# Kernel tuning notes

Hardware: AMD Instinct MI355X
Metric: run time of the kernel (lower is better)

The kernel has to match this reference:

```python
import jax, jax.numpy as jnp
import numpy as np

# Dimensions derived from Mamba.__init__: d_model=512 -> joint_latent=32, mamb_latent=D=640
NL, D, DIN, DS, DTR, DC = 4, 640, 1280, 16, 40, 4  # n_layer, d_model, d_inner, d_state, dt_rank, d_conv
B, V = 64, 30  # batch, joint-sequence length (repeat_joint_num)


def _rms(x, w, eps=1e-5):
    return x * jax.lax.rsqrt(jnp.mean(x * x, axis=-1, keepdims=True) + eps) * w


def _mamba_block(x, in_w, conv_w, conv_b, xp_w, dt_w, dt_b, A_log, D_skip, out_w):
    # x: [B, V, D]
    u, res = jnp.split(jnp.einsum('bvd,ed->bve', x, in_w), 2, axis=-1)  # each [B,V,DIN]
    # causal depthwise conv1d over V
    xc = jnp.pad(u.transpose(0, 2, 1), ((0, 0), (0, 0), (DC - 1, 0)))  # [B,DIN,V+DC-1]
    xc = jax.lax.conv_general_dilated(xc, conv_w[:, None, :], (1,), 'VALID',
                                      feature_group_count=DIN,
                                      dimension_numbers=('NCH', 'OIH', 'NCH'))
    u = jax.nn.silu(xc.transpose(0, 2, 1) + conv_b)  # [B,V,DIN]
    # input-dependent SSM params
    dbl = jnp.einsum('bvd,ed->bve', u, xp_w)  # [B,V,DTR+2*DS]
    delta, Bm, Cm = jnp.split(dbl, [DTR, DTR + DS], axis=-1)
    delta = jax.nn.softplus(jnp.einsum('bvr,dr->bvd', delta, dt_w) + dt_b)  # [B,V,DIN]
    A = -jnp.exp(A_log)  # [DIN,DS]
    dA = jnp.exp(delta[..., None] * A)                              # [B,V,DIN,DS]
    dBu = delta[..., None] * Bm[:, :, None, :] * u[..., None]       # [B,V,DIN,DS]

    def step(h, t):
        dA_t, dBu_t, C_t = t
        h = dA_t * h + dBu_t                      # [B,DIN,DS]
        return h, jnp.einsum('bds,bs->bd', h, C_t)

    h0 = jnp.zeros((x.shape[0], DIN, DS), x.dtype)
    _, ys = jax.lax.scan(step, h0, (dA.transpose(1, 0, 2, 3),
                                    dBu.transpose(1, 0, 2, 3),
                                    Cm.transpose(1, 0, 2)))
    y = ys.transpose(1, 0, 2) + u * D_skip        # [B,V,DIN]
    return jnp.einsum('bvd,ed->bve', y * jax.nn.silu(res), out_w)


def setup_inputs() -> dict:
    key = jax.random.key(0)
    ks = jax.random.split(key, 10)
    s = 0.02
    return {
        'x': jax.random.normal(ks[0], (B, V, D), jnp.float32),
        'vs': jax.random.randint(ks[1], (B,), 0, V),
        'norm_w': jnp.ones((NL, D), jnp.float32),
        'in_proj_w': s * jax.random.normal(ks[2], (NL, 2 * DIN, D), jnp.float32),
        'conv_w': s * jax.random.normal(ks[3], (NL, DIN, DC), jnp.float32),
        'conv_b': jnp.zeros((NL, DIN), jnp.float32),
        'x_proj_w': s * jax.random.normal(ks[4], (NL, DTR + 2 * DS, DIN), jnp.float32),
        'dt_proj_w': s * jax.random.normal(ks[5], (NL, DIN, DTR), jnp.float32),
        'dt_proj_b': jnp.full((NL, DIN), -4.0, jnp.float32) + 0.1 * jax.random.normal(ks[6], (NL, DIN), jnp.float32),
        'A_log': jnp.tile(jnp.log(jnp.arange(1.0, DS + 1.0, dtype=jnp.float32)), (NL, DIN, 1)),
        'D_skip': jnp.ones((NL, DIN), jnp.float32),
        'out_proj_w': s * jax.random.normal(ks[7], (NL, D, DIN), jnp.float32),
        'norm_f_w': jnp.ones((D,), jnp.float32),
    }


def reference(x, vs, norm_w, in_proj_w, conv_w, conv_b, x_proj_w, dt_proj_w,
              dt_proj_b, A_log, D_skip, out_proj_w, norm_f_w):
    bidx = jnp.arange(x.shape[0])[:, None]
    # batch-wise circular permutation over V (circular_permute_v)
    fwd_idx = (jnp.arange(V)[None, :] + V - vs[:, None]) % V  # [B,V]
    h = x[bidx, fwd_idx]
    for i in range(NL):
        h = h + _mamba_block(_rms(h, norm_w[i]), in_proj_w[i], conv_w[i], conv_b[i],
                             x_proj_w[i], dt_proj_w[i], dt_proj_b[i], A_log[i],
                             D_skip[i], out_proj_w[i])
    h = _rms(h, norm_f_w)
    # reverse_circular_permute_v
    rev_idx = (jnp.arange(V)[None, :] + vs[:, None]) % V
    return h[bidx, rev_idx]
```

## Files before the change

### kernel.cpp

```cpp
#include <hip/hip_runtime.h>
#include <math.h>

#define NLAYER 4
#define DMODEL 640
#define DINNER 1280
#define DSTATE 16
#define DTRANK 40
#define DCONV  4
#define BATCH  64
#define SEQ    30
#define MTOK   (BATCH*SEQ)
#define NPROJ  (2*DINNER)
#define NDBL   (DTRANK+2*DSTATE)
#define NDBLP  80
#define KSEGS  8
#define KSEG   (DINNER/KSEGS)
#define DTKP   64

#define Q1 (NLAYER*NPROJ*DMODEL/4)
#define Q2 (NLAYER*DMODEL*DINNER/4)
#define Q3 (NLAYER*NDBLP*DINNER/4)
#define Q4 (NLAYER*DINNER*DTKP/4)
#define WCTOT (Q1+Q2+Q3+Q4)

typedef unsigned short u16;
typedef __bf16 bf16x8 __attribute__((ext_vector_type(8)));
typedef float  f32x4  __attribute__((ext_vector_type(4)));
typedef unsigned short u16x8 __attribute__((ext_vector_type(8)));

__device__ __forceinline__ float siluf(float x) {
    return x / (1.0f + __expf(-x));
}

__device__ __forceinline__ u16 f2bf(float f) {
    unsigned int u = __float_as_uint(f);
    u += 0x7fffu + ((u >> 16) & 1u);
    return (u16)(u >> 16);
}

__device__ __forceinline__ float bf2f(u16 b) {
    return __uint_as_float(((unsigned int)b) << 16);
}

__global__ void k_permute(const float* __restrict__ x, const int* __restrict__ vs,
                          float* __restrict__ h) {
    int idx = blockIdx.x * blockDim.x + threadIdx.x;
    if (idx >= MTOK * DMODEL) return;
    int d  = idx % DMODEL;
    int mv = idx / DMODEL;
    int v  = mv % SEQ;
    int b  = mv / SEQ;
    int src = (v + SEQ - vs[b]) % SEQ;
    h[idx] = x[(b * SEQ + src) * DMODEL + d];
}

__global__ __launch_bounds__(256)
void k_wconv(const float* __restrict__ in_w, const float* __restrict__ out_w,
             const float* __restrict__ xp_w, const float* __restrict__ dt_w,
             u16* __restrict__ wbi, u16* __restrict__ wbo,
             u16* __restrict__ wbx, u16* __restrict__ wdt) {
    int i = blockIdx.x * 256 + threadIdx.x;
    if (i < Q1) {
        int j = i * 4;
        float4 v = *(const float4*)(in_w + j);
        ushort4 o;
        o.x = f2bf(v.x); o.y = f2bf(v.y); o.z = f2bf(v.z); o.w = f2bf(v.w);
        *(ushort4*)(wbi + j) = o;
    } else if (i < Q1 + Q2) {
        int j = (i - Q1) * 4;
        float4 v = *(const float4*)(out_w + j);
        ushort4 o;
        o.x = f2bf(v.x); o.y = f2bf(v.y); o.z = f2bf(v.z); o.w = f2bf(v.w);
        *(ushort4*)(wbo + j) = o;
    } else if (i < Q1 + Q2 + Q3) {
        int j = (i - Q1 - Q2) * 4;
        int layer = j / (NDBLP * DINNER);
        int rem   = j % (NDBLP * DINNER);
        int r = rem / DINNER, c = rem % DINNER;
        ushort4 o = make_ushort4(0, 0, 0, 0);
        if (r < NDBL) {
            float4 v = *(const float4*)(xp_w + ((size_t)layer * NDBL + r) * DINNER + c);
            o.x = f2bf(v.x); o.y = f2bf(v.y); o.z = f2bf(v.z); o.w = f2bf(v.w);
        }
        *(ushort4*)(wbx + j) = o;
    } else {
        int j = (i - Q1 - Q2 - Q3) * 4;
        int ld = j / DTKP;
        int c  = j % DTKP;
        ushort4 o = make_ushort4(0, 0, 0, 0);
        if (c < DTRANK) {
            float4 v = *(const float4*)(dt_w + (size_t)ld * DTRANK + c);
            o.x = f2bf(v.x); o.y = f2bf(v.y); o.z = f2bf(v.z); o.w = f2bf(v.w);
        }
        *(ushort4*)(wdt + j) = o;
    }
}

__global__ __launch_bounds__(64)
void k_rmsnorm(const float* __restrict__ h, const float* __restrict__ w,
               u16* __restrict__ xn) {
    int m = blockIdx.x;
    int t = threadIdx.x;
    const float* row = h + (size_t)m * DMODEL;
    float2 vv[5];
    float ss = 0.f;
    #pragma unroll
    for (int i = 0; i < 5; ++i) {
        vv[i] = *(const float2*)(row + i * 128 + t * 2);
        ss += vv[i].x * vv[i].x + vv[i].y * vv[i].y;
    }
    #pragma unroll
    for (int o = 32; o > 0; o >>= 1) ss += __shfl_xor(ss, o, 64);
    float sc = rsqrtf(ss / DMODEL + 1e-5f);
    u16* outp = xn + (size_t)m * DMODEL;
    #pragma unroll
    for (int i = 0; i < 5; ++i) {
        int d = i * 128 + t * 2;
        float2 wv = *(const float2*)(w + d);
        ushort2 o;
        o.x = f2bf(vv[i].x * sc * wv.x);
        o.y = f2bf(vv[i].y * sc * wv.y);
        *(ushort2*)(outp + d) = o;
    }
}

__global__ __launch_bounds__(256)
void k_inproj(const u16* __restrict__ A, const u16* __restrict__ W,
              u16* __restrict__ Cb) {
    __shared__ u16 As[2][64 * 64];
    __shared__ u16 Bs[2][128 * 64];
    const int t = threadIdx.x;
    const int w = t >> 6, l = t & 63;
    const int lane15 = l & 15, quad = l >> 4;
    const int wm = w >> 1, wn = w & 1;
    const int m0 = blockIdx.y * 64, n0 = blockIdx.x * 128;

    f32x4 acc[2][4];
    #pragma unroll
    for (int i = 0; i < 2; ++i)
        #pragma unroll
        for (int j = 0; j < 4; ++j)
            acc[i][j] = (f32x4){0.f, 0.f, 0.f, 0.f};

    auto stage = [&](int buf, int k0) {
        #pragma unroll
        for (int q = 0; q < 2; ++q) {
            int c   = q * 256 + t;
            int row = c >> 3;
            int gch = ((c & 7) ^ (row & 7)) * 8;
            const u16* ga = A + (size_t)(m0 + row) * DMODEL + k0 + gch;
            __builtin_amdgcn_global_load_lds(
                (const __attribute__((address_space(1))) void*)ga,
                (__attribute__((address_space(3))) void*)&As[buf][c * 8], 16, 0, 0);
        }
        #pragma unroll
        for (int q = 0; q < 4; ++q) {
            int c   = q * 256 + t;
            int row = c >> 3;
            int gch = ((c & 7) ^ (row & 7)) * 8;
            const u16* gb = W + (size_t)(n0 + row) * DMODEL + k0 + gch;
            __builtin_amdgcn_global_load_lds(
                (const __attribute__((address_space(1))) void*)gb,
                (__attribute__((address_space(3))) void*)&Bs[buf][c * 8], 16, 0, 0);
        }
    };

    auto compute = [&](int buf) {
        #pragma unroll
        for (int ks = 0; ks < 2; ++ks) {
            bf16x8 af[2], bfr[4];
            #pragma unroll
            for (int i = 0; i < 2; ++i) {
                int row = wm * 32 + i * 16 + lane15;
                af[i] = *(const bf16x8*)&As[buf][row * 64 + (((ks * 4 + quad) ^ (row & 7)) * 8)];
            }
            #pragma unroll
            for (int j = 0; j < 4; ++j) {
                int row = wn * 64 + j * 16 + lane15;
                bfr[j] = *(const bf16x8*)&Bs[buf][row * 64 + (((ks * 4 + quad) ^ (row & 7)) * 8)];
            }
            #pragma unroll
            for (int i = 0; i < 2; ++i)
                #pragma unroll
                for (int j = 0; j < 4; ++j)
                    acc[i][j] = __builtin_amdgcn_mfma_f32_16x16x32_bf16(
                        af[i], bfr[j], acc[i][j], 0, 0, 0);
        }
    };

    const int NT = DMODEL / 64;
    stage(0, 0);
    __syncthreads();
    int cur = 0;
    for (int tt = 1; tt < NT; ++tt) {
        stage(cur ^ 1, tt * 64);
        compute(cur);
        __syncthreads();
        cur ^= 1;
    }
    compute(cur);

    #pragma unroll
    for (int i = 0; i < 2; ++i) {
        #pragma unroll
        for (int r = 0; r < 4; ++r) {
            int row = m0 + wm * 32 + i * 16 + quad * 4 + r;
            #pragma unroll
            for (int j = 0; j < 4; ++j) {
                int col = n0 + wn * 64 + j * 16 + lane15;
                Cb[(size_t)row * NPROJ + col] = f2bf(acc[i][j][r]);
            }
        }
    }
}

__global__ __launch_bounds__(128)
void k_outproj(const u16* __restrict__ A, const u16* __restrict__ W,
               const float* __restrict__ resid, float* __restrict__ C) {
    __shared__ u16 As[2][32 * 64];
    __shared__ u16 Bs[2][64 * 64];
    const int t = threadIdx.x;
    const int w = t >> 6, l = t & 63;
    const int lane15 = l & 15, quad = l >> 4;
    const int m0 = blockIdx.y * 32, n0 = blockIdx.x * 64;

    f32x4 acc[2][2];
    #pragma unroll
    for (int i = 0; i < 2; ++i)
        #pragma unroll
        for (int j = 0; j < 2; ++j)
            acc[i][j] = (f32x4){0.f, 0.f, 0.f, 0.f};

    auto stage = [&](int buf, int k0) {
        #pragma unroll
        for (int q = 0; q < 2; ++q) {
            int c   = q * 128 + t;
            int row = c >> 3;
            int gch = ((c & 7) ^ (row & 7)) * 8;
            const u16* ga = A + (size_t)(m0 + row) * DINNER + k0 + gch;
            __builtin_amdgcn_global_load_lds(
                (const __attribute__((address_space(1))) void*)ga,
                (__attribute__((address_space(3))) void*)&As[buf][c * 8], 16, 0, 0);
        }
        #pragma unroll
        for (int q = 0; q < 4; ++q) {
            int c   = q * 128 + t;
            int row = c >> 3;
            int gch = ((c & 7) ^ (row & 7)) * 8;
            const u16* gb = W + (size_t)(n0 + row) * DINNER + k0 + gch;
            __builtin_amdgcn_global_load_lds(
                (const __attribute__((address_space(1))) void*)gb,
                (__attribute__((address_space(3))) void*)&Bs[buf][c * 8], 16, 0, 0);
        }
    };

    auto compute = [&](int buf) {
        #pragma unroll
        for (int ks = 0; ks < 2; ++ks) {
            bf16x8 af[2], bfr[2];
            #pragma unroll
            for (int i = 0; i < 2; ++i) {
                int row = i * 16 + lane15;
                af[i] = *(const bf16x8*)&As[buf][row * 64 + (((ks * 4 + quad) ^ (row & 7)) * 8)];
            }
            #pragma unroll
            for (int j = 0; j < 2; ++j) {
                int row = w * 32 + j * 16 + lane15;
                bfr[j] = *(const bf16x8*)&Bs[buf][row * 64 + (((ks * 4 + quad) ^ (row & 7)) * 8)];
            }
            #pragma unroll
            for (int i = 0; i < 2; ++i)
                #pragma unroll
                for (int j = 0; j < 2; ++j)
                    acc[i][j] = __builtin_amdgcn_mfma_f32_16x16x32_bf16(
                        af[i], bfr[j], acc[i][j], 0, 0, 0);
        }
    };

    const int NT = DINNER / 64;
    stage(0, 0);
    __syncthreads();
    int cur = 0;
    for (int tt = 1; tt < NT; ++tt) {
        stage(cur ^ 1, tt * 64);
        compute(cur);
        __syncthreads();
        cur ^= 1;
    }
    compute(cur);

    #pragma unroll
    for (int i = 0; i < 2; ++i) {
        #pragma unroll
        for (int r = 0; r < 4; ++r) {
            int row = m0 + i * 16 + quad * 4 + r;
            #pragma unroll
            for (int j = 0; j < 2; ++j) {
                int col = n0 + w * 32 + j * 16 + lane15;
                size_t idx = (size_t)row * DMODEL + col;
                C[idx] = acc[i][j][r] + resid[idx];
            }
        }
    }
}

__global__ __launch_bounds__(256)
void k_conv(const u16* __restrict__ urb, const float* __restrict__ cw,
            const float* __restrict__ cb, u16* __restrict__ ubf) {
    int idx = blockIdx.x * 256 + threadIdx.x;
    int c = idx % DINNER;
    int b = idx / DINNER;
    const u16* up = urb + (size_t)(b * SEQ) * NPROJ + c;
    float xv[SEQ];
    #pragma unroll
    for (int v = 0; v < SEQ; ++v) xv[v] = bf2f(up[(size_t)v * NPROJ]);
    float w0 = cw[c * 4 + 0], w1 = cw[c * 4 + 1];
    float w2 = cw[c * 4 + 2], w3 = cw[c * 4 + 3];
    float bias = cb[c];
    u16* op = ubf + (size_t)(b * SEQ) * DINNER + c;
    float x0 = 0.f, x1 = 0.f, x2 = 0.f;
    #pragma unroll
    for (int v = 0; v < SEQ; ++v) {
        float x3 = xv[v];
        float o = bias + w0 * x0 + w1 * x1 + w2 * x2 + w3 * x3;
        op[(size_t)v * DINNER] = f2bf(siluf(o));
        x0 = x1; x1 = x2; x2 = x3;
    }
}

__global__ __launch_bounds__(256)
void k_xproj(const u16* __restrict__ ubf, const u16* __restrict__ wbx,
             float* __restrict__ dblp) {
    __shared__ u16 As[64 * 32];
    __shared__ u16 Bs[NDBLP * 32];
    const int t = threadIdx.x;
    const int w = t >> 6, l = t & 63;
    const int lane15 = l & 15, quad = l >> 4;
    const int seg = blockIdx.x;
    const int m0 = blockIdx.y * 64;
    const int kb = seg * KSEG;

    f32x4 acc[5];
    #pragma unroll
    for (int j = 0; j < 5; ++j) acc[j] = (f32x4){0.f, 0.f, 0.f, 0.f};

    for (int k0 = 0; k0 < KSEG; k0 += 32) {
        __syncthreads();
        {
            int c = t;
            const u16* ga = ubf + (size_t)(m0 + (c >> 2)) * DINNER + kb + k0 + (c & 3) * 8;
            __builtin_amdgcn_global_load_lds(
                (const __attribute__((address_space(1))) void*)ga,
                (__attribute__((address_space(3))) void*)&As[c * 8], 16, 0, 0);
            const u16* gb = wbx + (size_t)(c >> 2) * DINNER + kb + k0 + (c & 3) * 8;
            __builtin_amdgcn_global_load_lds(
                (const __attribute__((address_space(1))) void*)gb,
                (__attribute__((address_space(3))) void*)&Bs[c * 8], 16, 0, 0);
        }
        if (t < 64) {
            int c = 256 + t;
            const u16* gb = wbx + (size_t)(c >> 2) * DINNER + kb + k0 + (c & 3) * 8;
            __builtin_amdgcn_global_load_lds(
                (const __attribute__((address_space(1))) void*)gb,
                (__attribute__((address_space(3))) void*)&Bs[c * 8], 16, 0, 0);
        }
        __syncthreads();

        bf16x8 af = *(const bf16x8*)&As[(w * 16 + lane15) * 32 + quad * 8];
        #pragma unroll
        for (int j = 0; j < 5; ++j) {
            bf16x8 bfrag = *(const bf16x8*)&Bs[(j * 16 + lane15) * 32 + quad * 8];
            acc[j] = __builtin_amdgcn_mfma_f32_16x16x32_bf16(af, bfrag, acc[j], 0, 0, 0);
        }
    }

    float* outp = dblp + (size_t)seg * MTOK * NDBLP;
    #pragma unroll
    for (int r = 0; r < 4; ++r) {
        int row = m0 + w * 16 + quad * 4 + r;
        #pragma unroll
        for (int j = 0; j < 5; ++j) {
            int col = j * 16 + lane15;
            outp[(size_t)row * NDBLP + col] = acc[j][r];
        }
    }
}

__global__ __launch_bounds__(256)
void k_dtgemm(const float* __restrict__ dblp, const u16* __restrict__ dtwb,
              const float* __restrict__ dtb, u16* __restrict__ delta) {
    __shared__ u16 As[64 * 32];
    __shared__ u16 Bs[64 * 32];
    const int t = threadIdx.x;
    const int w = t >> 6, l = t & 63;
    const int lane15 = l & 15, quad = l >> 4;
    const int wm = w >> 1, wn = w & 1;
    const int m0 = blockIdx.y * 64, n0 = blockIdx.x * 64;
    const int row = t >> 2, koff = (t & 3) * 8;
    const int m = m0 + row;

    f32x4 acc[2][2];
    #pragma unroll
    for (int i = 0; i < 2; ++i)
        #pragma unroll
        for (int j = 0; j < 2; ++j)
            acc[i][j] = (f32x4){0.f, 0.f, 0.f, 0.f};

    #pragma unroll
    for (int k0 = 0; k0 < DTKP; k0 += 32) {
        float sums[8] = {0.f, 0.f, 0.f, 0.f, 0.f, 0.f, 0.f, 0.f};
        #pragma unroll
        for (int q = 0; q < 2; ++q) {
            int col = k0 + koff + q * 4;
            if (col < DTRANK) {
                #pragma unroll
                for (int sg = 0; sg < KSEGS; ++sg) {
                    float4 p = *(const float4*)&dblp[(size_t)sg * MTOK * NDBLP
                                                     + (size_t)m * NDBLP + col];
                    sums[q * 4 + 0] += p.x; sums[q * 4 + 1] += p.y;
                    sums[q * 4 + 2] += p.z; sums[q * 4 + 3] += p.w;
                }
            }
        }
        u16x8 av;
        #pragma unroll
        for (int e = 0; e < 8; ++e) av[e] = f2bf(sums[e]);
        __syncthreads();
        *(u16x8*)&As[row * 32 + koff] = av;
        {
            int c = t;
            const u16* gb = dtwb + (size_t)(n0 + (c >> 2)) * DTKP + k0 + (c & 3) * 8;
            __builtin_amdgcn_global_load_lds(
                (const __attribute__((address_space(1))) void*)gb,
                (__attribute__((address_space(3))) void*)&Bs[c * 8], 16, 0, 0);
        }
        __syncthreads();

        bf16x8 af[2], bfrag[2];
        #pragma unroll
        for (int i = 0; i < 2; ++i)
            af[i] = *(const bf16x8*)&As[(wm * 32 + i * 16 + lane15) * 32 + quad * 8];
        #pragma unroll
        for (int j = 0; j < 2; ++j)
            bfrag[j] = *(const bf16x8*)&Bs[(wn * 32 + j * 16 + lane15) * 32 + quad * 8];
        #pragma unroll
        for (int i = 0; i < 2; ++i)
            #pragma unroll
            for (int j = 0; j < 2; ++j)
                acc[i][j] = __builtin_amdgcn_mfma_f32_16x16x32_bf16(
                    af[i], bfrag[j], acc[i][j], 0, 0, 0);
    }

    #pragma unroll
    for (int i = 0; i < 2; ++i) {
        #pragma unroll
        for (int r = 0; r < 4; ++r) {
            int orow = m0 + wm * 32 + i * 16 + quad * 4 + r;
            #pragma unroll
            for (int j = 0; j < 2; ++j) {
                int col = n0 + wn * 32 + j * 16 + lane15;
                float vv = acc[i][j][r] + dtb[col];
                vv = (vv > 20.f) ? vv : log1pf(__expf(vv));
                delta[(size_t)orow * DINNER + col] = f2bf(vv);
            }
        }
    }
}

__global__ __launch_bounds__(256)
void k_scan(const u16* __restrict__ ubf, const u16* __restrict__ urb,
            const float* __restrict__ dblp, const u16* __restrict__ delta,
            const float* __restrict__ A_log, const float* __restrict__ Dsk,
            u16* __restrict__ y) {
    __shared__ float BC[SEQ][2 * DSTATE];
    const int b  = blockIdx.x / (DINNER / 256);
    const int dc = blockIdx.x % (DINNER / 256);
    const int d  = dc * 256 + threadIdx.x;

    for (int t = threadIdx.x; t < SEQ * 2 * DSTATE; t += 256) {
        int v = t >> 5, s = t & 31;
        float acc = 0.f;
        #pragma unroll
        for (int sg = 0; sg < KSEGS; ++sg)
            acc += dblp[(size_t)sg * MTOK * NDBLP + (size_t)(b * SEQ + v) * NDBLP + DTRANK + s];
        BC[v][s] = acc;
    }
    __syncthreads();

    float dl[SEQ], uu[SEQ], rr[SEQ];
    #pragma unroll
    for (int v = 0; v < SEQ; ++v)
        dl[v] = bf2f(delta[(size_t)(b * SEQ + v) * DINNER + d]);
    #pragma unroll
    for (int v = 0; v < SEQ; ++v)
        uu[v] = bf2f(ubf[(size_t)(b * SEQ + v) * DINNER + d]);
    #pragma unroll
    for (int v = 0; v < SEQ; ++v)
        rr[v] = bf2f(urb[(size_t)(b * SEQ + v) * NPROJ + DINNER + d]);

    float Ar[DSTATE];
    #pragma unroll
    for (int s = 0; s < DSTATE; ++s) Ar[s] = -__expf(A_log[(size_t)d * DSTATE + s]);
    float dsk = Dsk[d];
    float st[DSTATE];
    #pragma unroll
    for (int s = 0; s < DSTATE; ++s) st[s] = 0.f;

    u16* yp = y + (size_t)(b * SEQ) * DINNER + d;

    #pragma unroll
    for (int v = 0; v < SEQ; ++v) {
        float dlt = dl[v];
        float du  = dlt * uu[v];
        float ya0 = 0.f, ya1 = 0.f, ya2 = 0.f, ya3 = 0.f;
        #pragma unroll
        for (int s = 0; s < DSTATE; s += 4) {
            float dA0 = __expf(dlt * Ar[s + 0]);
            float dA1 = __expf(dlt * Ar[s + 1]);
            float dA2 = __expf(dlt * Ar[s + 2]);
            float dA3 = __expf(dlt * Ar[s + 3]);
            st[s + 0] = dA0 * st[s + 0] + du * BC[v][s + 0];
            st[s + 1] = dA1 * st[s + 1] + du * BC[v][s + 1];
            st[s + 2] = dA2 * st[s + 2] + du * BC[v][s + 2];
            st[s + 3] = dA3 * st[s + 3] + du * BC[v][s + 3];
            ya0 += st[s + 0] * BC[v][DSTATE + s + 0];
            ya1 += st[s + 1] * BC[v][DSTATE + s + 1];
            ya2 += st[s + 2] * BC[v][DSTATE + s + 2];
            ya3 += st[s + 3] * BC[v][DSTATE + s + 3];
        }
        float ya = (ya0 + ya1) + (ya2 + ya3);
        yp[(size_t)v * DINNER] = f2bf((ya + uu[v] * dsk) * siluf(rr[v]));
    }
}

__global__ __launch_bounds__(64)
void k_final(const float* __restrict__ h, const int* __restrict__ vs,
             const float* __restrict__ w, float* __restrict__ out) {
    int mv = blockIdx.x;
    int v = mv % SEQ, b = mv / SEQ;
    int src = (v + vs[b]) % SEQ;
    const float* row = h + (size_t)(b * SEQ + src) * DMODEL;
    int t = threadIdx.x;
    float ss = 0.f;
    for (int d = t; d < DMODEL; d += 64) { float x = row[d]; ss += x * x; }
    #pragma unroll
    for (int o = 32; o > 0; o >>= 1) ss += __shfl_xor(ss, o, 64);
    float sc = rsqrtf(ss / DMODEL + 1e-5f);
    float* op = out + (size_t)mv * DMODEL;
    for (int d = t; d < DMODEL; d += 64) op[d] = row[d] * sc * w[d];
}

extern "C" void kernel_launch(void* const* d_in, const int* in_sizes, int n_in,
                              void* d_out, int out_size, void* d_ws, size_t ws_size,
                              hipStream_t stream) {
    const float* x      = (const float*)d_in[0];
    const int*   vs     = (const int*)d_in[1];
    const float* norm_w = (const float*)d_in[2];
    const float* in_w   = (const float*)d_in[3];
    const float* conv_w = (const float*)d_in[4];
    const float* conv_b = (const float*)d_in[5];
    const float* xp_w   = (const float*)d_in[6];
    const float* dt_w   = (const float*)d_in[7];
    const float* dt_b   = (const float*)d_in[8];
    const float* A_log  = (const float*)d_in[9];
    const float* Dsk    = (const float*)d_in[10];
    const float* out_w  = (const float*)d_in[11];
    const float* nfw    = (const float*)d_in[12];
    float* out = (float*)d_out;

    char* p = (char*)d_ws;
    float* h      = (float*)p; p += (size_t)MTOK * DMODEL * 4;
    u16*   xn     = (u16*)p;   p += (size_t)MTOK * DMODEL * 2;
    u16*   urb    = (u16*)p;   p += (size_t)MTOK * NPROJ * 2;
    u16*   ubf    = (u16*)p;   p += (size_t)MTOK * DINNER * 2;
    float* dblp   = (float*)p; p += (size_t)KSEGS * MTOK * NDBLP * 4;
    u16*   deltab = (u16*)p;   p += (size_t)MTOK * DINNER * 2;
    u16*   y      = (u16*)p;   p += (size_t)MTOK * DINNER * 2;
    u16*   wbi4   = (u16*)p;   p += (size_t)NLAYER * NPROJ * DMODEL * 2;
    u16*   wbo4   = (u16*)p;   p += (size_t)NLAYER * DMODEL * DINNER * 2;
    u16*   wbx4   = (u16*)p;   p += (size_t)NLAYER * NDBLP * DINNER * 2;
    u16*   wdt4   = (u16*)p;   p += (size_t)NLAYER * DINNER * DTKP * 2;

    k_wconv<<<WCTOT / 256, 256, 0, stream>>>(
        in_w, out_w, xp_w, dt_w, wbi4, wbo4, wbx4, wdt4);

    k_permute<<<(MTOK * DMODEL + 255) / 256, 256, 0, stream>>>(x, vs, h);

    for (int l = 0; l < NLAYER; ++l) {
        k_rmsnorm<<<MTOK, 64, 0, stream>>>(h, norm_w + (size_t)l * DMODEL, xn);

        k_inproj<<<dim3(NPROJ / 128, MTOK / 64), 256, 0, stream>>>(
            xn, wbi4 + (size_t)l * NPROJ * DMODEL, urb);

        k_conv<<<BATCH * DINNER / 256, 256, 0, stream>>>(
            urb, conv_w + (size_t)l * DINNER * DCONV, conv_b + (size_t)l * DINNER, ubf);

        k_xproj<<<dim3(KSEGS, MTOK / 64), 256, 0, stream>>>(
            ubf, wbx4 + (size_t)l * NDBLP * DINNER, dblp);

        k_dtgemm<<<dim3(DINNER / 64, MTOK / 64), 256, 0, stream>>>(
            dblp, wdt4 + (size_t)l * DINNER * DTKP,
            dt_b + (size_t)l * DINNER, deltab);

        k_scan<<<BATCH * (DINNER / 256), 256, 0, stream>>>(
            ubf, urb, dblp, deltab,
            A_log + (size_t)l * DINNER * DSTATE, Dsk + (size_t)l * DINNER, y);

        k_outproj<<<dim3(DMODEL / 64, MTOK / 32), 128, 0, stream>>>(
            y, wbo4 + (size_t)l * DMODEL * DINNER, h, h);
    }

    k_final<<<MTOK, 64, 0, stream>>>(h, vs, nfw, out);
}
```

Before: 464.6 us.

## Fuse RMSNorm into in_proj GEMM via sum-of-squares from out_proj epilogue

Removes the per-layer RMSNorm kernel. The out_proj epilogue now accumulates each row's sum of squares into a buffer with atomics, and in_proj loads the fp32 residual, applies the scale and norm weight, converts to bf16 and writes it into LDS itself. The permute kernel and the weight conversion are merged into one pre-kernel that also computes the first layer's sum of squares and zeroes the later per-layer buffers. This saves a launch and a bf16 round trip per layer, but in_proj now reads fp32 activations through registers instead of the async global-to-LDS copy, and the atomics add contention.

```diff
diff --git a/kernel.cpp b/kernel.cpp
--- a/kernel.cpp
+++ b/kernel.cpp
@@ -22,6 +22,9 @@
 #define Q3 (NLAYER*NDBLP*DINNER/4)
 #define Q4 (NLAYER*DINNER*DTKP/4)
 #define WCTOT (Q1+Q2+Q3+Q4)
+#define WCBLK (WCTOT/256)
+#define PERMB (MTOK/4)
+#define ZBLK  30
 
 typedef unsigned short u16;
 typedef __bf16 bf16x8 __attribute__((ext_vector_type(8)));
@@ -42,117 +45,123 @@
     return __uint_as_float(((unsigned int)b) << 16);
 }
 
-__global__ void k_permute(const float* __restrict__ x, const int* __restrict__ vs,
-                          float* __restrict__ h) {
-    int idx = blockIdx.x * blockDim.x + threadIdx.x;
-    if (idx >= MTOK * DMODEL) return;
-    int d  = idx % DMODEL;
-    int mv = idx / DMODEL;
-    int v  = mv % SEQ;
-    int b  = mv / SEQ;
-    int src = (v + SEQ - vs[b]) % SEQ;
-    h[idx] = x[(b * SEQ + src) * DMODEL + d];
-}
-
 __global__ __launch_bounds__(256)
-void k_wconv(const float* __restrict__ in_w, const float* __restrict__ out_w,
-             const float* __restrict__ xp_w, const float* __restrict__ dt_w,
-             u16* __restrict__ wbi, u16* __restrict__ wbo,
-             u16* __restrict__ wbx, u16* __restrict__ wdt) {
-    int i = blockIdx.x * 256 + threadIdx.x;
-    if (i < Q1) {
-        int j = i * 4;
-        float4 v = *(const float4*)(in_w + j);
-        ushort4 o;
-        o.x = f2bf(v.x); o.y = f2bf(v.y); o.z = f2bf(v.z); o.w = f2bf(v.w);
-        *(ushort4*)(wbi + j) = o;
-    } else if (i < Q1 + Q2) {
-        int j = (i - Q1) * 4;
-        float4 v = *(const float4*)(out_w + j);
-        ushort4 o;
-        o.x = f2bf(v.x); o.y = f2bf(v.y); o.z = f2bf(v.z); o.w = f2bf(v.w);
-        *(ushort4*)(wbo + j) = o;
-    } else if (i < Q1 + Q2 + Q3) {
-        int j = (i - Q1 - Q2) * 4;
-        int layer = j / (NDBLP * DINNER);
-        int rem   = j % (NDBLP * DINNER);
-        int r = rem / DINNER, c = rem % DINNER;
-        ushort4 o = make_ushort4(0, 0, 0, 0);
-        if (r < NDBL) {
-            float4 v = *(const float4*)(xp_w + ((size_t)layer * NDBL + r) * DINNER + c);
+void k_pre(const float* __restrict__ in_w, const float* __restrict__ out_w,
+           const float* __restrict__ xp_w, const float* __restrict__ dt_w,
+           u16* __restrict__ wbi, u16* __restrict__ wbo,
+           u16* __restrict__ wbx, u16* __restrict__ wdt,
+           const float* __restrict__ x, const int* __restrict__ vs,
+           float* __restrict__ h, float* __restrict__ ssq) {
+    int bid = blockIdx.x;
+    int t = threadIdx.x;
+    if (bid < WCBLK) {
+        int i = bid * 256 + t;
+        if (i < Q1) {
+            int j = i * 4;
+            float4 v = *(const float4*)(in_w + j);
+            ushort4 o;
             o.x = f2bf(v.x); o.y = f2bf(v.y); o.z = f2bf(v.z); o.w = f2bf(v.w);
-        }
-        *(ushort4*)(wbx + j) = o;
+            *(ushort4*)(wbi + j) = o;
+        } else if (i < Q1 + Q2) {
+            int j = (i - Q1) * 4;
+            float4 v = *(const float4*)(out_w + j);
+            ushort4 o;
+            o.x = f2bf(v.x); o.y = f2bf(v.y); o.z = f2bf(v.z); o.w = f2bf(v.w);
+            *(ushort4*)(wbo + j) = o;
+        } else if (i < Q1 + Q2 + Q3) {
+            int j = (i - Q1 - Q2) * 4;
+            int layer = j / (NDBLP * DINNER);
+            int rem   = j % (NDBLP * DINNER);
+            int r = rem / DINNER, c = rem % DINNER;
+            ushort4 o = make_ushort4(0, 0, 0, 0);
+            if (r < NDBL) {
+                float4 v = *(const float4*)(xp_w + ((size_t)layer * NDBL + r) * DINNER + c);
+                o.x = f2bf(v.x); o.y = f2bf(v.y); o.z = f2bf(v.z); o.w = f2bf(v.w);
+            }
+            *(ushort4*)(wbx + j) = o;
+        } else {
+            int j = (i - Q1 - Q2 - Q3) * 4;
+            int ld = j / DTKP;
+            int c  = j % DTKP;
+            ushort4 o = make_ushort4(0, 0, 0, 0);
+            if (c < DTRANK) {
+                float4 v = *(const float4*)(dt_w + (size_t)ld * DTRANK + c);
+                o.x = f2bf(v.x); o.y = f2bf(v.y); o.z = f2bf(v.z); o.w = f2bf(v.w);
+            }
+            *(ushort4*)(wdt + j) = o;
+        }
+    } else if (bid < WCBLK + PERMB) {
+        int rb = bid - WCBLK;
+        int wv = t >> 6, lane = t & 63;
+        int mv = rb * 4 + wv;
+        int v = mv % SEQ, b = mv / SEQ;
+        int src = (v + SEQ - vs[b]) % SEQ;
+        const float* xr = x + (size_t)(b * SEQ + src) * DMODEL;
+        float* hr = h + (size_t)mv * DMODEL;
+        float2 vv[5];
+        float ss = 0.f;
+        #pragma unroll
+        for (int i = 0; i < 5; ++i) {
+            vv[i] = *(const float2*)(xr + i * 128 + lane * 2);
+            ss += vv[i].x * vv[i].x + vv[i].y * vv[i].y;
+        }
+        #pragma unroll
+        for (int o = 32; o > 0; o >>= 1) ss += __shfl_xor(ss, o, 64);
+        #pragma unroll
+        for (int i = 0; i < 5; ++i)
+            *(float2*)(hr + i * 128 + lane * 2) = vv[i];
+        if (lane == 0) ssq[mv] = ss;
     } else {
-        int j = (i - Q1 - Q2 - Q3) * 4;
-        int ld = j / DTKP;
-        int c  = j % DTKP;
-        ushort4 o = make_ushort4(0, 0, 0, 0);
-        if (c < DTRANK) {
-            float4 v = *(const float4*)(dt_w + (size_t)ld * DTRANK + c);
-            o.x = f2bf(v.x); o.y = f2bf(v.y); o.z = f2bf(v.z); o.w = f2bf(v.w);
-        }
-        *(ushort4*)(wdt + j) = o;
-    }
-}
-
-__global__ __launch_bounds__(64)
-void k_rmsnorm(const float* __restrict__ h, const float* __restrict__ w,
-               u16* __restrict__ xn) {
-    int m = blockIdx.x;
-    int t = threadIdx.x;
-    const float* row = h + (size_t)m * DMODEL;
-    float2 vv[5];
-    float ss = 0.f;
-    #pragma unroll
-    for (int i = 0; i < 5; ++i) {
-        vv[i] = *(const float2*)(row + i * 128 + t * 2);
-        ss += vv[i].x * vv[i].x + vv[i].y * vv[i].y;
-    }
-    #pragma unroll
-    for (int o = 32; o > 0; o >>= 1) ss += __shfl_xor(ss, o, 64);
-    float sc = rsqrtf(ss / DMODEL + 1e-5f);
-    u16* outp = xn + (size_t)m * DMODEL;
-    #pragma unroll
-    for (int i = 0; i < 5; ++i) {
-        int d = i * 128 + t * 2;
-        float2 wv = *(const float2*)(w + d);
-        ushort2 o;
-        o.x = f2bf(vv[i].x * sc * wv.x);
-        o.y = f2bf(vv[i].y * sc * wv.y);
-        *(ushort2*)(outp + d) = o;
+        int idx = (bid - WCBLK - PERMB) * 256 + t;
+        if (idx < 4 * MTOK) ssq[MTOK + idx] = 0.f;
     }
 }
 
 __global__ __launch_bounds__(256)
-void k_inproj(const u16* __restrict__ A, const u16* __restrict__ W,
-              u16* __restrict__ Cb) {
+void k_inproj(const float* __restrict__ h, const float* __restrict__ ssq,
+              const float* __restrict__ nw,
+              const u16* __restrict__ W, u16* __restrict__ Cb) {
     __shared__ u16 As[2][64 * 64];
     __shared__ u16 Bs[2][128 * 64];
+    __shared__ float nws[DMODEL];
     const int t = threadIdx.x;
     const int w = t >> 6, l = t & 63;
     const int lane15 = l & 15, quad = l >> 4;
     const int wm = w >> 1, wn = w & 1;
     const int m0 = blockIdx.y * 64, n0 = blockIdx.x * 128;
 
-    f32x4 acc[2][4];
-    #pragma unroll
-    for (int i = 0; i < 2; ++i)
-        #pragma unroll
-        for (int j = 0; j < 4; ++j)
-            acc[i][j] = (f32x4){0.f, 0.f, 0.f, 0.f};
-
-    auto stage = [&](int buf, int k0) {
-        #pragma unroll
-        for (int q = 0; q < 2; ++q) {
-            int c   = q * 256 + t;
-            int row = c >> 3;
-            int gch = ((c & 7) ^ (row & 7)) * 8;
-            const u16* ga = A + (size_t)(m0 + row) * DMODEL + k0 + gch;
-            __builtin_amdgcn_global_load_lds(
-                (const __attribute__((address_space(1))) void*)ga,
-                (__attribute__((address_space(3))) void*)&As[buf][c * 8], 16, 0, 0);
-        }
+    {
+        int i4 = t;
+        if (i4 < DMODEL / 4)
+            *(float4*)&nws[i4 * 4] = *(const float4*)&nw[i4 * 4];
+        if (i4 + 256 < DMODEL / 4) {}
+    }
+
+    const int arow = t >> 2, akoff = (t & 3) * 16;
+    const float ascale = rsqrtf(ssq[m0 + arow] / DMODEL + 1e-5f);
+
+    f32x4 a0, a1, a2, a3;
+    auto loadA = [&](int k0) {
+        const float* hp = h + (size_t)(m0 + arow) * DMODEL + k0 + akoff;
+        a0 = *(const f32x4*)hp;       a1 = *(const f32x4*)(hp + 4);
+        a2 = *(const f32x4*)(hp + 8); a3 = *(const f32x4*)(hp + 12);
+    };
+    auto writeA = [&](int buf, int k0) {
+        const float* wp = &nws[k0 + akoff];
+        u16x8 o0, o1;
+        o0[0] = f2bf(a0[0] * ascale * wp[0]);  o0[1] = f2bf(a0[1] * ascale * wp[1]);
+        o0[2] = f2bf(a0[2] * ascale * wp[2]);  o0[3] = f2bf(a0[3] * ascale * wp[3]);
+        o0[4] = f2bf(a1[0] * ascale * wp[4]);  o0[5] = f2bf(a1[1] * ascale * wp[5]);
+        o0[6] = f2bf(a1[2] * ascale * wp[6]);  o0[7] = f2bf(a1[3] * ascale * wp[7]);
+        o1[0] = f2bf(a2[0] * ascale * wp[8]);  o1[1] = f2bf(a2[1] * ascale * wp[9]);
+        o1[2] = f2bf(a2[2] * ascale * wp[10]); o1[3] = f2bf(a2[3] * ascale * wp[11]);
+        o1[4] = f2bf(a3[0] * ascale * wp[12]); o1[5] = f2bf(a3[1] * ascale * wp[13]);
+        o1[6] = f2bf(a3[2] * ascale * wp[14]); o1[7] = f2bf(a3[3] * ascale * wp[15]);
+        int ch0 = (t & 3) * 2;
+        *(u16x8*)&As[buf][arow * 64 + ((ch0 ^ (arow & 7)) * 8)] = o0;
+        *(u16x8*)&As[buf][arow * 64 + (((ch0 + 1) ^ (arow & 7)) * 8)] = o1;
+    };
+    auto stageB = [&](int buf, int k0) {
         #pragma unroll
         for (int q = 0; q < 4; ++q) {
             int c   = q * 256 + t;
@@ -165,6 +174,13 @@
         }
     };
 
+    f32x4 acc[2][4];
+    #pragma unroll
+    for (int i = 0; i < 2; ++i)
+        #pragma unroll
+        for (int j = 0; j < 4; ++j)
+            acc[i][j] = (f32x4){0.f, 0.f, 0.f, 0.f};
+
     auto compute = [&](int buf) {
         #pragma unroll
         for (int ks = 0; ks < 2; ++ks) {
@@ -189,12 +205,17 @@
     };
 
     const int NT = DMODEL / 64;
-    stage(0, 0);
+    loadA(0);
+    stageB(0, 0);
+    __syncthreads();
+    writeA(0, 0);
     __syncthreads();
     int cur = 0;
     for (int tt = 1; tt < NT; ++tt) {
-        stage(cur ^ 1, tt * 64);
+        loadA(tt * 64);
+        stageB(cur ^ 1, tt * 64);
         compute(cur);
+        writeA(cur ^ 1, tt * 64);
         __syncthreads();
         cur ^= 1;
     }
@@ -216,7 +237,8 @@
 
 __global__ __launch_bounds__(128)
 void k_outproj(const u16* __restrict__ A, const u16* __restrict__ W,
-               const float* __restrict__ resid, float* __restrict__ C) {
+               const float* __restrict__ resid, float* __restrict__ C,
+               float* __restrict__ ssqn) {
     __shared__ u16 As[2][32 * 64];
     __shared__ u16 Bs[2][64 * 64];
     const int t = threadIdx.x;
@@ -289,6 +311,7 @@
     }
     compute(cur);
 
+    float hv[2][4][2];
     #pragma unroll
     for (int i = 0; i < 2; ++i) {
         #pragma unroll
@@ -298,8 +321,21 @@
             for (int j = 0; j < 2; ++j) {
                 int col = n0 + w * 32 + j * 16 + lane15;
                 size_t idx = (size_t)row * DMODEL + col;
-                C[idx] = acc[i][j][r] + resid[idx];
-            }
+                float v = acc[i][j][r] + resid[idx];
+                C[idx] = v;
+                hv[i][r][j] = v;
+            }
+        }
+    }
+    #pragma unroll
+    for (int i = 0; i < 2; ++i) {
+        #pragma unroll
+        for (int r = 0; r < 4; ++r) {
+            float p = hv[i][r][0] * hv[i][r][0] + hv[i][r][1] * hv[i][r][1];
+            #pragma unroll
+            for (int o = 1; o < 16; o <<= 1) p += __shfl_xor(p, o, 64);
+            if (lane15 == 0)
+                atomicAdd(&ssqn[m0 + i * 16 + quad * 4 + r], p);
         }
     }
 }
@@ -570,7 +606,7 @@
 
     char* p = (char*)d_ws;
     float* h      = (float*)p; p += (size_t)MTOK * DMODEL * 4;
-    u16*   xn     = (u16*)p;   p += (size_t)MTOK * DMODEL * 2;
+    float* ssq    = (float*)p; p += (size_t)5 * MTOK * 4;
     u16*   urb    = (u16*)p;   p += (size_t)MTOK * NPROJ * 2;
     u16*   ubf    = (u16*)p;   p += (size_t)MTOK * DINNER * 2;
     float* dblp   = (float*)p; p += (size_t)KSEGS * MTOK * NDBLP * 4;
@@ -581,16 +617,13 @@
     u16*   wbx4   = (u16*)p;   p += (size_t)NLAYER * NDBLP * DINNER * 2;
     u16*   wdt4   = (u16*)p;   p += (size_t)NLAYER * DINNER * DTKP * 2;
 
-    k_wconv<<<WCTOT / 256, 256, 0, stream>>>(
-        in_w, out_w, xp_w, dt_w, wbi4, wbo4, wbx4, wdt4);
-
-    k_permute<<<(MTOK * DMODEL + 255) / 256, 256, 0, stream>>>(x, vs, h);
+    k_pre<<<WCBLK + PERMB + ZBLK, 256, 0, stream>>>(
+        in_w, out_w, xp_w, dt_w, wbi4, wbo4, wbx4, wdt4, x, vs, h, ssq);
 
     for (int l = 0; l < NLAYER; ++l) {
-        k_rmsnorm<<<MTOK, 64, 0, stream>>>(h, norm_w + (size_t)l * DMODEL, xn);
-
         k_inproj<<<dim3(NPROJ / 128, MTOK / 64), 256, 0, stream>>>(
-            xn, wbi4 + (size_t)l * NPROJ * DMODEL, urb);
+            h, ssq + (size_t)l * MTOK, norm_w + (size_t)l * DMODEL,
+            wbi4 + (size_t)l * NPROJ * DMODEL, urb);
 
         k_conv<<<BATCH * DINNER / 256, 256, 0, stream>>>(
             urb, conv_w + (size_t)l * DINNER * DCONV, conv_b + (size_t)l * DINNER, ubf);
@@ -607,7 +640,8 @@
             A_log + (size_t)l * DINNER * DSTATE, Dsk + (size_t)l * DINNER, y);
 
         k_outproj<<<dim3(DMODEL / 64, MTOK / 32), 128, 0, stream>>>(
-            y, wbo4 + (size_t)l * DMODEL * DINNER, h, h);
+            y, wbo4 + (size_t)l * DMODEL * DINNER, h, h,
+            ssq + (size_t)(l + 1) * MTOK);
     }
 
     k_final<<<MTOK, 64, 0, stream>>>(h, vs, nfw, out);
```

Result: slower. 487.0 us (+4.8%).

## Double-buffer xproj LDS, batch dtgemm loads, split scan state across lane pairs

Applied to the files above, without the earlier changes.

k_xproj now double-buffers its LDS tiles, so the next K-slice is fetched while MFMAs run on the current one. k_dtgemm loads both K tiles up front and needs a single barrier instead of two per iteration. k_scan splits the 16 SSM states across two lanes per channel and combines the partial outputs with a shuffle, doubling the grid to raise parallelism and cut per-thread serial work. In exchange, each lane pair loads the same per-channel delta/u/res values twice, LDS use rises, and every second lane sits idle at the store.

```diff
diff --git a/kernel.cpp b/kernel.cpp
--- a/kernel.cpp
+++ b/kernel.cpp
@@ -331,8 +331,8 @@
 __global__ __launch_bounds__(256)
 void k_xproj(const u16* __restrict__ ubf, const u16* __restrict__ wbx,
              float* __restrict__ dblp) {
-    __shared__ u16 As[64 * 32];
-    __shared__ u16 Bs[NDBLP * 32];
+    __shared__ u16 As[2][64 * 32];
+    __shared__ u16 Bs[2][NDBLP * 32];
     const int t = threadIdx.x;
     const int w = t >> 6, l = t & 63;
     const int lane15 = l & 15, quad = l >> 4;
@@ -344,35 +344,46 @@
     #pragma unroll
     for (int j = 0; j < 5; ++j) acc[j] = (f32x4){0.f, 0.f, 0.f, 0.f};
 
-    for (int k0 = 0; k0 < KSEG; k0 += 32) {
-        __syncthreads();
+    auto stage = [&](int buf, int k0) {
         {
             int c = t;
             const u16* ga = ubf + (size_t)(m0 + (c >> 2)) * DINNER + kb + k0 + (c & 3) * 8;
             __builtin_amdgcn_global_load_lds(
                 (const __attribute__((address_space(1))) void*)ga,
-                (__attribute__((address_space(3))) void*)&As[c * 8], 16, 0, 0);
+                (__attribute__((address_space(3))) void*)&As[buf][c * 8], 16, 0, 0);
             const u16* gb = wbx + (size_t)(c >> 2) * DINNER + kb + k0 + (c & 3) * 8;
             __builtin_amdgcn_global_load_lds(
                 (const __attribute__((address_space(1))) void*)gb,
-                (__attribute__((address_space(3))) void*)&Bs[c * 8], 16, 0, 0);
+                (__attribute__((address_space(3))) void*)&Bs[buf][c * 8], 16, 0, 0);
         }
         if (t < 64) {
             int c = 256 + t;
             const u16* gb = wbx + (size_t)(c >> 2) * DINNER + kb + k0 + (c & 3) * 8;
             __builtin_amdgcn_global_load_lds(
                 (const __attribute__((address_space(1))) void*)gb,
-                (__attribute__((address_space(3))) void*)&Bs[c * 8], 16, 0, 0);
-        }
+                (__attribute__((address_space(3))) void*)&Bs[buf][c * 8], 16, 0, 0);
+        }
+    };
+
+    auto compute = [&](int buf) {
+        bf16x8 af = *(const bf16x8*)&As[buf][(w * 16 + lane15) * 32 + quad * 8];
+        #pragma unroll
+        for (int j = 0; j < 5; ++j) {
+            bf16x8 bfrag = *(const bf16x8*)&Bs[buf][(j * 16 + lane15) * 32 + quad * 8];
+            acc[j] = __builtin_amdgcn_mfma_f32_16x16x32_bf16(af, bfrag, acc[j], 0, 0, 0);
+        }
+    };
+
+    stage(0, 0);
+    __syncthreads();
+    int cur = 0;
+    for (int k0 = 32; k0 < KSEG; k0 += 32) {
+        stage(cur ^ 1, k0);
+        compute(cur);
         __syncthreads();
-
-        bf16x8 af = *(const bf16x8*)&As[(w * 16 + lane15) * 32 + quad * 8];
-        #pragma unroll
-        for (int j = 0; j < 5; ++j) {
-            bf16x8 bfrag = *(const bf16x8*)&Bs[(j * 16 + lane15) * 32 + quad * 8];
-            acc[j] = __builtin_amdgcn_mfma_f32_16x16x32_bf16(af, bfrag, acc[j], 0, 0, 0);
-        }
-    }
+        cur ^= 1;
+    }
+    compute(cur);
 
     float* outp = dblp + (size_t)seg * MTOK * NDBLP;
     #pragma unroll
@@ -389,8 +400,8 @@
 __global__ __launch_bounds__(256)
 void k_dtgemm(const float* __restrict__ dblp, const u16* __restrict__ dtwb,
               const float* __restrict__ dtb, u16* __restrict__ delta) {
-    __shared__ u16 As[64 * 32];
-    __shared__ u16 Bs[64 * 32];
+    __shared__ u16 As[2][64 * 32];
+    __shared__ u16 Bs[2][64 * 32];
     const int t = threadIdx.x;
     const int w = t >> 6, l = t & 63;
     const int lane15 = l & 15, quad = l >> 4;
@@ -399,50 +410,61 @@
     const int row = t >> 2, koff = (t & 3) * 8;
     const int m = m0 + row;
 
-    f32x4 acc[2][2];
-    #pragma unroll
-    for (int i = 0; i < 2; ++i)
-        #pragma unroll
-        for (int j = 0; j < 2; ++j)
-            acc[i][j] = (f32x4){0.f, 0.f, 0.f, 0.f};
-
-    #pragma unroll
-    for (int k0 = 0; k0 < DTKP; k0 += 32) {
-        float sums[8] = {0.f, 0.f, 0.f, 0.f, 0.f, 0.f, 0.f, 0.f};
+    #pragma unroll
+    for (int kt = 0; kt < 2; ++kt) {
+        int c = t;
+        const u16* gb = dtwb + (size_t)(n0 + (c >> 2)) * DTKP + kt * 32 + (c & 3) * 8;
+        __builtin_amdgcn_global_load_lds(
+            (const __attribute__((address_space(1))) void*)gb,
+            (__attribute__((address_space(3))) void*)&Bs[kt][c * 8], 16, 0, 0);
+    }
+
+    float sums[2][8];
+    #pragma unroll
+    for (int kt = 0; kt < 2; ++kt)
+        #pragma unroll
+        for (int e = 0; e < 8; ++e) sums[kt][e] = 0.f;
+    #pragma unroll
+    for (int kt = 0; kt < 2; ++kt) {
         #pragma unroll
         for (int q = 0; q < 2; ++q) {
-            int col = k0 + koff + q * 4;
+            int col = kt * 32 + koff + q * 4;
             if (col < DTRANK) {
                 #pragma unroll
                 for (int sg = 0; sg < KSEGS; ++sg) {
                     float4 p = *(const float4*)&dblp[(size_t)sg * MTOK * NDBLP
                                                      + (size_t)m * NDBLP + col];
-                    sums[q * 4 + 0] += p.x; sums[q * 4 + 1] += p.y;
-                    sums[q * 4 + 2] += p.z; sums[q * 4 + 3] += p.w;
+                    sums[kt][q * 4 + 0] += p.x; sums[kt][q * 4 + 1] += p.y;
+                    sums[kt][q * 4 + 2] += p.z; sums[kt][q * 4 + 3] += p.w;
                 }
             }
         }
+    }
+    #pragma unroll
+    for (int kt = 0; kt < 2; ++kt) {
         u16x8 av;
         #pragma unroll
-        for (int e = 0; e < 8; ++e) av[e] = f2bf(sums[e]);
-        __syncthreads();
-        *(u16x8*)&As[row * 32 + koff] = av;
-        {
-            int c = t;
-            const u16* gb = dtwb + (size_t)(n0 + (c >> 2)) * DTKP + k0 + (c & 3) * 8;
-            __builtin_amdgcn_global_load_lds(
-                (const __attribute__((address_space(1))) void*)gb,
-                (__attribute__((address_space(3))) void*)&Bs[c * 8], 16, 0, 0);
-        }
-        __syncthreads();
-
+        for (int e = 0; e < 8; ++e) av[e] = f2bf(sums[kt][e]);
+        *(u16x8*)&As[kt][row * 32 + koff] = av;
+    }
+    __syncthreads();
+
+    f32x4 acc[2][2];
+    #pragma unroll
+    for (int i = 0; i < 2; ++i)
+        #pragma unroll
+        for (int j = 0; j < 2; ++j)
+            acc[i][j] = (f32x4){0.f, 0.f, 0.f, 0.f};
+
+    #pragma unroll
+    for (int kt = 0; kt < 2; ++kt) {
         bf16x8 af[2], bfrag[2];
         #pragma unroll
         for (int i = 0; i < 2; ++i)
-            af[i] = *(const bf16x8*)&As[(wm * 32 + i * 16 + lane15) * 32 + quad * 8];
+            af[i] = *(const bf16x8*)&As[kt][(wm * 32 + i * 16 + lane15) * 32 + quad * 8];
         #pragma unroll
         for (int j = 0; j < 2; ++j)
-            bfrag[j] = *(const bf16x8*)&Bs[(wn * 32 + j * 16 + lane15) * 32 + quad * 8];
+            bfrag[j] = *(const bf16x8*)&Bs[kt][(wn * 32 + j * 16 + lane15) * 32 + quad * 8];
         #pragma unroll
         for (int i = 0; i < 2; ++i)
             #pragma unroll
@@ -473,9 +495,11 @@
             const float* __restrict__ A_log, const float* __restrict__ Dsk,
             u16* __restrict__ y) {
     __shared__ float BC[SEQ][2 * DSTATE];
-    const int b  = blockIdx.x / (DINNER / 256);
-    const int dc = blockIdx.x % (DINNER / 256);
-    const int d  = dc * 256 + threadIdx.x;
+    const int b  = blockIdx.x / (DINNER / 128);
+    const int dc = blockIdx.x % (DINNER / 128);
+    const int dloc = threadIdx.x >> 1;
+    const int half = threadIdx.x & 1;
+    const int d  = dc * 128 + dloc;
 
     for (int t = threadIdx.x; t < SEQ * 2 * DSTATE; t += 256) {
         int v = t >> 5, s = t & 31;
@@ -498,13 +522,14 @@
     for (int v = 0; v < SEQ; ++v)
         rr[v] = bf2f(urb[(size_t)(b * SEQ + v) * NPROJ + DINNER + d]);
 
-    float Ar[DSTATE];
-    #pragma unroll
-    for (int s = 0; s < DSTATE; ++s) Ar[s] = -__expf(A_log[(size_t)d * DSTATE + s]);
+    float Ar[8];
+    #pragma unroll
+    for (int s = 0; s < 8; ++s)
+        Ar[s] = -__expf(A_log[(size_t)d * DSTATE + half * 8 + s]);
     float dsk = Dsk[d];
-    float st[DSTATE];
-    #pragma unroll
-    for (int s = 0; s < DSTATE; ++s) st[s] = 0.f;
+    float st8[8];
+    #pragma unroll
+    for (int s = 0; s < 8; ++s) st8[s] = 0.f;
 
     u16* yp = y + (size_t)(b * SEQ) * DINNER + d;
 
@@ -512,24 +537,26 @@
     for (int v = 0; v < SEQ; ++v) {
         float dlt = dl[v];
         float du  = dlt * uu[v];
-        float ya0 = 0.f, ya1 = 0.f, ya2 = 0.f, ya3 = 0.f;
-        #pragma unroll
-        for (int s = 0; s < DSTATE; s += 4) {
+        float ya = 0.f, yb = 0.f;
+        #pragma unroll
+        for (int s = 0; s < 8; s += 4) {
             float dA0 = __expf(dlt * Ar[s + 0]);
             float dA1 = __expf(dlt * Ar[s + 1]);
             float dA2 = __expf(dlt * Ar[s + 2]);
             float dA3 = __expf(dlt * Ar[s + 3]);
-            st[s + 0] = dA0 * st[s + 0] + du * BC[v][s + 0];
-            st[s + 1] = dA1 * st[s + 1] + du * BC[v][s + 1];
-            st[s + 2] = dA2 * st[s + 2] + du * BC[v][s + 2];
-            st[s + 3] = dA3 * st[s + 3] + du * BC[v][s + 3];
-            ya0 += st[s + 0] * BC[v][DSTATE + s + 0];
-            ya1 += st[s + 1] * BC[v][DSTATE + s + 1];
-            ya2 += st[s + 2] * BC[v][DSTATE + s + 2];
-            ya3 += st[s + 3] * BC[v][DSTATE + s + 3];
-        }
-        float ya = (ya0 + ya1) + (ya2 + ya3);
-        yp[(size_t)v * DINNER] = f2bf((ya + uu[v] * dsk) * siluf(rr[v]));
+            st8[s + 0] = dA0 * st8[s + 0] + du * BC[v][half * 8 + s + 0];
+            st8[s + 1] = dA1 * st8[s + 1] + du * BC[v][half * 8 + s + 1];
+            st8[s + 2] = dA2 * st8[s + 2] + du * BC[v][half * 8 + s + 2];
+            st8[s + 3] = dA3 * st8[s + 3] + du * BC[v][half * 8 + s + 3];
+            ya += st8[s + 0] * BC[v][DSTATE + half * 8 + s + 0];
+            yb += st8[s + 1] * BC[v][DSTATE + half * 8 + s + 1];
+            ya += st8[s + 2] * BC[v][DSTATE + half * 8 + s + 2];
+            yb += st8[s + 3] * BC[v][DSTATE + half * 8 + s + 3];
+        }
+        float yh = ya + yb;
+        yh += __shfl_xor(yh, 1, 64);
+        if (half == 0)
+            yp[(size_t)v * DINNER] = f2bf((yh + uu[v] * dsk) * siluf(rr[v]));
     }
 }
 
@@ -602,7 +629,7 @@
             dblp, wdt4 + (size_t)l * DINNER * DTKP,
             dt_b + (size_t)l * DINNER, deltab);
 
-        k_scan<<<BATCH * (DINNER / 256), 256, 0, stream>>>(
+        k_scan<<<BATCH * (DINNER / 128), 256, 0, stream>>>(
             ubf, urb, dblp, deltab,
             A_log + (size_t)l * DINNER * DSTATE, Dsk + (size_t)l * DINNER, y);
 
```

Measured after the change: 454.4 us. 1.02x faster.
